# Optimization experiments

Measured on AMD Instinct MI355X. Metric: run time of the kernel, lower is better.

The kernel has to match this reference:

```python
import jax, jax.numpy as jnp
import numpy as np

N, E, F_IN = 12288, 196608, 1433


def setup_inputs() -> dict:
    key = jax.random.key(0)
    ks = jax.random.split(key, 11)
    inp = {
        "x": jax.random.normal(ks[0], (N, F_IN), dtype=jnp.float32),
        "edge_index": jax.random.randint(ks[1], (2, E), 0, N, dtype=jnp.int64),
        "W1": jax.random.normal(ks[2], (F_IN, 32), dtype=jnp.float32) * 0.02,
        "b1": jnp.zeros((32,), dtype=jnp.float32),
        "Wl": jax.random.normal(ks[3], (32, 16), dtype=jnp.float32) * 0.1,
        "bl": jnp.zeros((16,), dtype=jnp.float32),
        "Wr": jax.random.normal(ks[4], (32, 16), dtype=jnp.float32) * 0.1,
        "br": jnp.zeros((16,), dtype=jnp.float32),
        "W3": jax.random.normal(ks[5], (16, 7), dtype=jnp.float32) * 0.1,
        "b3": jnp.zeros((7,), dtype=jnp.float32),
    }
    return inp


def reference(x, edge_index, W1, b1, Wl, bl, Wr, br, W3, b3):
    n = x.shape[0]
    loops = jnp.arange(n, dtype=edge_index.dtype)
    row = jnp.concatenate([edge_index[0], loops])  # [E+N]
    col = jnp.concatenate([edge_index[1], loops])

    # ---- GCN layer: dense symmetric-normalized adjacency (faithful to original) ----
    # degree computed over the col index of self-looped edges
    deg = jnp.zeros((n,), dtype=x.dtype).at[col].add(1.0)
    dis = jnp.where(deg > 0, deg ** -0.5, 0.0)  # inf -> 0 guard
    A = jnp.zeros((n, n), dtype=x.dtype).at[row, col].add(1.0)  # dense A-hat
    A_norm = dis[:, None] * A * dis[None, :]  # D^-1/2 A D^-1/2
    h = (A_norm @ x) @ W1 + b1
    h = jax.nn.relu(h)  # [N, 32]

    # ---- GraphSAGE layer: mean over neighbors j with edge (i -> j) ----
    src, dst = edge_index[0], edge_index[1]
    agg_sum = jax.ops.segment_sum(h[dst], src, num_segments=n)  # [N, 32]
    cnt = jax.ops.segment_sum(jnp.ones((src.shape[0],), dtype=h.dtype), src, num_segments=n)
    agg = jnp.where(cnt[:, None] > 0, agg_sum / jnp.maximum(cnt, 1.0)[:, None], 0.0)
    out = jax.nn.relu(h @ Wl + bl + agg @ Wr + br)  # [N, 16]
    out = out / (jnp.linalg.norm(out, axis=1, keepdims=True) + 1e-6)

    # ---- head: linear + dropout(eval: identity) + softmax ----
    logits = out @ W3 + b3  # [N, 7]
    return jax.nn.softmax(logits, axis=1)
```

## Files before the change

### kernel.cpp

```cpp
#include <hip/hip_runtime.h>
#include <hip/hip_bf16.h>
#include <math.h>

#define GN 12288
#define GE 196608
#define GK 1433
#define GC 32
#define CAP 64
#define NGRP 192
#define GEMMB 768
#define EDGEB 768
#define PACKB 24
#define ZEROB 96
#define XSTR2 260

typedef __attribute__((ext_vector_type(8))) short bf16x8;
typedef __attribute__((ext_vector_type(4))) float f32x4;
typedef float f32x4a __attribute__((ext_vector_type(4), aligned(4)));

static __device__ inline unsigned short f2bf(float f) {
    unsigned u = __float_as_uint(f);
    return (unsigned short)((u + 0x7fffu + ((u >> 16) & 1u)) >> 16);
}
static __device__ inline float bf2f(unsigned short h) {
    return __uint_as_float(((unsigned)h) << 16);
}
static __device__ inline unsigned short f2bf_hw(float f) {
    return __builtin_bit_cast(unsigned short, __float2bfloat16(f));
}

__global__ __launch_bounds__(256) void prep_kernel(const float* __restrict__ W1,
                                                   unsigned* __restrict__ zbuf,
                                                   unsigned short* __restrict__ Whb,
                                                   unsigned short* __restrict__ Wlb) {
    int t = threadIdx.x, b = blockIdx.x;
    if (b < PACKB) {
        int idx = b * 256 + t;
        int g = idx >> 5, c = idx & 31;
        bf16x8 vh, vl;
        #pragma unroll
        for (int j = 0; j < 8; ++j) {
            int k = g * 8 + j;
            float f = (k < GK) ? W1[(size_t)k * GC + c] : 0.f;
            unsigned short hh = f2bf(f);
            vh[j] = (short)hh;
            vl[j] = (short)f2bf(f - bf2f(hh));
        }
        *(bf16x8*)(Whb + (size_t)idx * 8) = vh;
        *(bf16x8*)(Wlb + (size_t)idx * 8) = vl;
    } else {
        int idx = (b - PACKB) * 256 + t;
        zbuf[idx] = 0u;
    }
}

__global__ __launch_bounds__(256) void fused_kernel(const float* __restrict__ x,
                                                    const int* __restrict__ ei,
                                                    const unsigned short* __restrict__ Whb,
                                                    const unsigned short* __restrict__ Wlb,
                                                    float* __restrict__ xw,
                                                    unsigned* __restrict__ cnt,
                                                    unsigned* __restrict__ deg,
                                                    unsigned* __restrict__ adjF) {
    int t = threadIdx.x, bid = blockIdx.x;

    if (bid >= GEMMB) {
        int e = (bid - GEMMB) * 256 + t;
        int src = ei[e];
        int dst = ei[GE + e];
        unsigned pos = atomicAdd(&cnt[src], 1u);
        if (pos < CAP) adjF[(unsigned)src * CAP + pos] = (unsigned)dst;
        atomicAdd(&deg[dst], 1u);
        return;
    }

    __shared__ __align__(16) float smem[2 * 16 * XSTR2];
    float (*xs)[16][XSTR2] = (float (*)[16][XSTR2])smem;
    int lane = t & 63, w = t >> 6;
    int quad = lane >> 4, l15 = lane & 15;
    const float* xb = x + (size_t)bid * 16 * GK;
    f32x4 acc0 = {}, acc1 = {};
    int r0w = t >> 6;
    int posc = t & 63;
    f32x4 gA0, gA1, gA2, gA3, gB0, gB1, gB2, gB3;

#define LOADG(G0, G1, G2, G3, S) { \
    const float* pp = xb + (size_t)r0w * GK + (S) * 256 + posc * 4; \
    G0 = *(const f32x4a*)(pp); \
    G1 = *(const f32x4a*)(pp + 4 * GK); \
    G2 = *(const f32x4a*)(pp + 8 * GK); \
    G3 = *(const f32x4a*)(pp + 12 * GK); }

#define LG1(DST, ROFF, PP, KB) { \
    const float* q_ = (PP) + (size_t)(ROFF) * GK; \
    if ((KB) + 4 <= GK) DST = *(const f32x4a*)q_; \
    else { \
        DST[0] = ((KB) + 0 < GK) ? q_[0] : 0.f; \
        DST[1] = ((KB) + 1 < GK) ? q_[1] : 0.f; \
        DST[2] = ((KB) + 2 < GK) ? q_[2] : 0.f; \
        DST[3] = ((KB) + 3 < GK) ? q_[3] : 0.f; } }

#define LOADGT(G0, G1, G2, G3, S) { \
    const float* pp = xb + (size_t)r0w * GK + (S) * 256 + posc * 4; \
    int kb = (S) * 256 + posc * 4; \
    LG1(G0, 0, pp, kb)  LG1(G1, 4, pp, kb)  LG1(G2, 8, pp, kb)  LG1(G3, 12, pp, kb) }

#define STOREL(G0, G1, G2, G3, BUF) { \
    float* lp = &xs[BUF][r0w][posc * 4]; \
    *(f32x4*)(lp)               = G0; \
    *(f32x4*)(lp + 4 * XSTR2)   = G1; \
    *(f32x4*)(lp + 8 * XSTR2)   = G2; \
    *(f32x4*)(lp + 12 * XSTR2)  = G3; }

#define COMPUTE(S, BUF) { \
    _Pragma("unroll") \
    for (int c = 0; c < 2; ++c) { \
        int kl = w * 64 + c * 32 + quad * 8; \
        const float* ap = &xs[BUF][l15][kl]; \
        f32x4 x0 = *(const f32x4*)ap; \
        f32x4 x1 = *(const f32x4*)(ap + 4); \
        bf16x8 ah, al; \
        _Pragma("unroll") for (int j = 0; j < 4; ++j) { \
            unsigned short hh = f2bf_hw(x0[j]); \
            ah[j] = (short)hh; al[j] = (short)f2bf_hw(x0[j] - bf2f(hh)); } \
        _Pragma("unroll") for (int j = 0; j < 4; ++j) { \
            unsigned short hh = f2bf_hw(x1[j]); \
            ah[4 + j] = (short)hh; al[4 + j] = (short)f2bf_hw(x1[j] - bf2f(hh)); } \
        int gg = (S) * 32 + w * 8 + c * 4 + quad; \
        bf16x8 H0 = *(const bf16x8*)(Whb + (size_t)gg * 256 + l15 * 8); \
        bf16x8 H1 = *(const bf16x8*)(Whb + (size_t)gg * 256 + 128 + l15 * 8); \
        bf16x8 L0 = *(const bf16x8*)(Wlb + (size_t)gg * 256 + l15 * 8); \
        bf16x8 L1 = *(const bf16x8*)(Wlb + (size_t)gg * 256 + 128 + l15 * 8); \
        acc0 = __builtin_amdgcn_mfma_f32_16x16x32_bf16(ah, H0, acc0, 0, 0, 0); \
        acc1 = __builtin_amdgcn_mfma_f32_16x16x32_bf16(ah, H1, acc1, 0, 0, 0); \
        acc0 = __builtin_amdgcn_mfma_f32_16x16x32_bf16(ah, L0, acc0, 0, 0, 0); \
        acc1 = __builtin_amdgcn_mfma_f32_16x16x32_bf16(ah, L1, acc1, 0, 0, 0); \
        acc0 = __builtin_amdgcn_mfma_f32_16x16x32_bf16(al, H0, acc0, 0, 0, 0); \
        acc1 = __builtin_amdgcn_mfma_f32_16x16x32_bf16(al, H1, acc1, 0, 0, 0); \
    } }

    LOADG(gA0, gA1, gA2, gA3, 0);
    STOREL(gA0, gA1, gA2, gA3, 0);
    LOADG(gB0, gB1, gB2, gB3, 1);
    __syncthreads();
    LOADG(gA0, gA1, gA2, gA3, 2);
    COMPUTE(0, 0);
    STOREL(gB0, gB1, gB2, gB3, 1);
    __syncthreads();
    LOADG(gB0, gB1, gB2, gB3, 3);
    COMPUTE(1, 1);
    STOREL(gA0, gA1, gA2, gA3, 0);
    __syncthreads();
    LOADG(gA0, gA1, gA2, gA3, 4);
    COMPUTE(2, 0);
    STOREL(gB0, gB1, gB2, gB3, 1);
    __syncthreads();
    LOADGT(gB0, gB1, gB2, gB3, 5);
    COMPUTE(3, 1);
    STOREL(gA0, gA1, gA2, gA3, 0);
    __syncthreads();
    COMPUTE(4, 0);
    STOREL(gB0, gB1, gB2, gB3, 1);
    __syncthreads();
    COMPUTE(5, 1);

    float (*red)[16][32] = (float (*)[16][32])smem;
    #pragma unroll
    for (int i = 0; i < 4; ++i) {
        red[w][quad * 4 + i][l15] = acc0[i];
        red[w][quad * 4 + i][16 + l15] = acc1[i];
    }
    __syncthreads();
    int rr0 = t >> 5, cc0 = t & 31;
    float s0 = red[0][rr0][cc0] + red[1][rr0][cc0] + red[2][rr0][cc0] + red[3][rr0][cc0];
    int rr1 = rr0 + 8;
    float s1 = red[0][rr1][cc0] + red[1][rr1][cc0] + red[2][rr1][cc0] + red[3][rr1][cc0];
    xw[(size_t)bid * 512 + t] = s0;
    xw[(size_t)bid * 512 + 256 + t] = s1;
}

__global__ __launch_bounds__(256) void gcn_kernel(const float* __restrict__ xw,
                                                  const unsigned* __restrict__ deg,
                                                  const unsigned* __restrict__ cnt,
                                                  const unsigned* __restrict__ adjF,
                                                  const float* __restrict__ b1,
                                                  float* __restrict__ h) {
    int w = threadIdx.x >> 6;
    int lane = threadIdx.x & 63;
    int i = blockIdx.x * 4 + w;
    int f = lane & 31, half = lane >> 5;
    unsigned cl = min(cnt[i], (unsigned)CAP);
    const unsigned* ai = adjF + (unsigned)i * CAP;
    float acc = 0.f;
    for (unsigned j = half; j < cl; j += 8) {
        unsigned lim = cl - 1;
        unsigned j1 = j + 2, j2 = j + 4, j3 = j + 6;
        unsigned d0 = ai[j];
        unsigned d1 = ai[min(j1, lim)];
        unsigned d2 = ai[min(j2, lim)];
        unsigned d3 = ai[min(j3, lim)];
        float m1 = j1 < cl ? 1.f : 0.f;
        float m2 = j2 < cl ? 1.f : 0.f;
        float m3 = j3 < cl ? 1.f : 0.f;
        acc += xw[(size_t)d0 * GC + f] * rsqrtf((float)(deg[d0] + 1u));
        acc += m1 * xw[(size_t)d1 * GC + f] * rsqrtf((float)(deg[d1] + 1u));
        acc += m2 * xw[(size_t)d2 * GC + f] * rsqrtf((float)(deg[d2] + 1u));
        acc += m3 * xw[(size_t)d3 * GC + f] * rsqrtf((float)(deg[d3] + 1u));
    }
    acc += __shfl_xor(acc, 32, 64);
    float disi = rsqrtf((float)(deg[i] + 1u));
    float v = b1[f] + disi * (disi * xw[(size_t)i * GC + f] + acc);
    if (half == 0) h[(size_t)i * GC + f] = fmaxf(v, 0.f);
}

__global__ __launch_bounds__(256) void sage_kernel(const float* __restrict__ h,
                                                   const unsigned* __restrict__ cnt,
                                                   const unsigned* __restrict__ adjF,
                                                   const float* __restrict__ Wl,
                                                   const float* __restrict__ bl,
                                                   const float* __restrict__ Wr,
                                                   const float* __restrict__ br,
                                                   const float* __restrict__ W3,
                                                   const float* __restrict__ b3,
                                                   float* __restrict__ out) {
    __shared__ float sh[4][64];
    __shared__ float so[4][16];
    int w = threadIdx.x >> 6, lane = threadIdx.x & 63;
    int i = blockIdx.x * 4 + w;
    int f = lane & 31, half = lane >> 5;
    unsigned ci = cnt[i];
    unsigned cl = min(ci, (unsigned)CAP);
    const unsigned* ai = adjF + (unsigned)i * CAP;
    float acc = 0.f;
    for (unsigned j = half; j < cl; j += 8) {
        unsigned lim = cl - 1;
        unsigned j1 = j + 2, j2 = j + 4, j3 = j + 6;
        unsigned d0 = ai[j];
        unsigned d1 = ai[min(j1, lim)];
        unsigned d2 = ai[min(j2, lim)];
        unsigned d3 = ai[min(j3, lim)];
        float m1 = j1 < cl ? 1.f : 0.f;
        float m2 = j2 < cl ? 1.f : 0.f;
        float m3 = j3 < cl ? 1.f : 0.f;
        acc += h[(size_t)d0 * GC + f];
        acc += m1 * h[(size_t)d1 * GC + f];
        acc += m2 * h[(size_t)d2 * GC + f];
        acc += m3 * h[(size_t)d3 * GC + f];
    }
    acc += __shfl_xor(acc, 32, 64);
    float agg = ci ? acc / (float)ci : 0.f;
    float hv = h[(size_t)i * GC + f];
    if (half == 0) { sh[w][f] = hv; sh[w][32 + f] = agg; }
    __syncthreads();
    int c = lane;
    float hid = 0.f;
    if (c < 16) {
        hid = bl[c] + br[c];
        #pragma unroll
        for (int ff = 0; ff < 32; ++ff)
            hid += sh[w][ff] * Wl[ff * 16 + c] + sh[w][32 + ff] * Wr[ff * 16 + c];
        hid = fmaxf(hid, 0.f);
    }
    float n2 = hid * hid;
    n2 += __shfl_xor(n2, 1, 64);
    n2 += __shfl_xor(n2, 2, 64);
    n2 += __shfl_xor(n2, 4, 64);
    n2 += __shfl_xor(n2, 8, 64);
    float o = hid / (sqrtf(n2) + 1e-6f);
    if (c < 16) so[w][c] = o;
    __syncthreads();
    float logit = -INFINITY;
    if (lane < 7) {
        logit = b3[lane];
        #pragma unroll
        for (int cc = 0; cc < 16; ++cc) logit += so[w][cc] * W3[cc * 7 + lane];
    }
    float m = logit;
    m = fmaxf(m, __shfl_xor(m, 1, 64));
    m = fmaxf(m, __shfl_xor(m, 2, 64));
    m = fmaxf(m, __shfl_xor(m, 4, 64));
    float e = expf(logit - m);
    float s = e;
    s += __shfl_xor(s, 1, 64);
    s += __shfl_xor(s, 2, 64);
    s += __shfl_xor(s, 4, 64);
    if (lane < 7) out[(size_t)i * 7 + lane] = e / s;
}

extern "C" void kernel_launch(void* const* d_in, const int* in_sizes, int n_in,
                              void* d_out, int out_size, void* d_ws, size_t ws_size,
                              hipStream_t stream) {
    const float* x  = (const float*)d_in[0];
    const int*   ei = (const int*)d_in[1];
    const float* W1 = (const float*)d_in[2];
    const float* b1 = (const float*)d_in[3];
    const float* Wl = (const float*)d_in[4];
    const float* bl = (const float*)d_in[5];
    const float* Wr = (const float*)d_in[6];
    const float* br = (const float*)d_in[7];
    const float* W3 = (const float*)d_in[8];
    const float* b3 = (const float*)d_in[9];
    float* out = (float*)d_out;

    char* ws = (char*)d_ws;
    const size_t S = (size_t)GN * GC * 4;
    float*    xw   = (float*)(ws);
    unsigned* cnt  = (unsigned*)(ws + S);
    unsigned* deg  = cnt + GN;
    float*    h    = (float*)(deg + GN);
    unsigned* adjF = (unsigned*)((char*)h + S);
    unsigned short* Whb = (unsigned short*)((char*)adjF + (size_t)GN * CAP * 4);
    unsigned short* Wlb = Whb + (size_t)NGRP * GC * 8;

    prep_kernel<<<PACKB + ZEROB, 256, 0, stream>>>(W1, cnt, Whb, Wlb);
    fused_kernel<<<GEMMB + EDGEB, 256, 0, stream>>>(x, ei, Whb, Wlb, xw, cnt, deg, adjF);
    gcn_kernel<<<GN / 4, 256, 0, stream>>>(xw, deg, cnt, adjF, b1, h);
    sage_kernel<<<GN / 4, 256, 0, stream>>>(h, cnt, adjF, Wl, bl, Wr, br, W3, b3, out);
}
```

Measured before the change: 153.6 us.

## Halve GEMM K-stage width to shrink LDS and deepen pipeline; memset counters

The x·W1 GEMM now streams K in 128-wide stages over 12 steps instead of 256-wide stages over 6 steps. Each thread holds two float4 registers per buffer instead of four, and the LDS tile shrinks by half. The aim is to cut shared memory and register pressure so more blocks fit on each CU and hide global-load latency better, at the cost of twice as many barriers. The counter zeroing moves from extra prep_kernel blocks to a hipMemsetAsync, which adds a separate stream operation.

```diff
diff --git a/kernel.cpp b/kernel.cpp
--- a/kernel.cpp
+++ b/kernel.cpp
@@ -11,8 +11,7 @@
 #define GEMMB 768
 #define EDGEB 768
 #define PACKB 24
-#define ZEROB 96
-#define XSTR2 260
+#define XSTR3 132
 
 typedef __attribute__((ext_vector_type(8))) short bf16x8;
 typedef __attribute__((ext_vector_type(4))) float f32x4;
@@ -30,28 +29,22 @@
 }
 
 __global__ __launch_bounds__(256) void prep_kernel(const float* __restrict__ W1,
-                                                   unsigned* __restrict__ zbuf,
                                                    unsigned short* __restrict__ Whb,
                                                    unsigned short* __restrict__ Wlb) {
     int t = threadIdx.x, b = blockIdx.x;
-    if (b < PACKB) {
-        int idx = b * 256 + t;
-        int g = idx >> 5, c = idx & 31;
-        bf16x8 vh, vl;
-        #pragma unroll
-        for (int j = 0; j < 8; ++j) {
-            int k = g * 8 + j;
-            float f = (k < GK) ? W1[(size_t)k * GC + c] : 0.f;
-            unsigned short hh = f2bf(f);
-            vh[j] = (short)hh;
-            vl[j] = (short)f2bf(f - bf2f(hh));
-        }
-        *(bf16x8*)(Whb + (size_t)idx * 8) = vh;
-        *(bf16x8*)(Wlb + (size_t)idx * 8) = vl;
-    } else {
-        int idx = (b - PACKB) * 256 + t;
-        zbuf[idx] = 0u;
-    }
+    int idx = b * 256 + t;
+    int g = idx >> 5, c = idx & 31;
+    bf16x8 vh, vl;
+    #pragma unroll
+    for (int j = 0; j < 8; ++j) {
+        int k = g * 8 + j;
+        float f = (k < GK) ? W1[(size_t)k * GC + c] : 0.f;
+        unsigned short hh = f2bf(f);
+        vh[j] = (short)hh;
+        vl[j] = (short)f2bf(f - bf2f(hh));
+    }
+    *(bf16x8*)(Whb + (size_t)idx * 8) = vh;
+    *(bf16x8*)(Wlb + (size_t)idx * 8) = vl;
 }
 
 __global__ __launch_bounds__(256) void fused_kernel(const float* __restrict__ x,
@@ -74,22 +67,20 @@
         return;
     }
 
-    __shared__ __align__(16) float smem[2 * 16 * XSTR2];
-    float (*xs)[16][XSTR2] = (float (*)[16][XSTR2])smem;
+    __shared__ __align__(16) float smem[2 * 16 * XSTR3];
+    float (*xs)[16][XSTR3] = (float (*)[16][XSTR3])smem;
     int lane = t & 63, w = t >> 6;
     int quad = lane >> 4, l15 = lane & 15;
     const float* xb = x + (size_t)bid * 16 * GK;
     f32x4 acc0 = {}, acc1 = {};
-    int r0w = t >> 6;
-    int posc = t & 63;
-    f32x4 gA0, gA1, gA2, gA3, gB0, gB1, gB2, gB3;
-
-#define LOADG(G0, G1, G2, G3, S) { \
-    const float* pp = xb + (size_t)r0w * GK + (S) * 256 + posc * 4; \
+    int row0 = t >> 5;
+    int posc = t & 31;
+    f32x4 gA0, gA1, gB0, gB1;
+
+#define LOADG(G0, G1, S) { \
+    const float* pp = xb + (size_t)row0 * GK + (S) * 128 + posc * 4; \
     G0 = *(const f32x4a*)(pp); \
-    G1 = *(const f32x4a*)(pp + 4 * GK); \
-    G2 = *(const f32x4a*)(pp + 8 * GK); \
-    G3 = *(const f32x4a*)(pp + 12 * GK); }
+    G1 = *(const f32x4a*)(pp + 8 * GK); }
 
 #define LG1(DST, ROFF, PP, KB) { \
     const float* q_ = (PP) + (size_t)(ROFF) * GK; \
@@ -100,70 +91,58 @@
         DST[2] = ((KB) + 2 < GK) ? q_[2] : 0.f; \
         DST[3] = ((KB) + 3 < GK) ? q_[3] : 0.f; } }
 
-#define LOADGT(G0, G1, G2, G3, S) { \
-    const float* pp = xb + (size_t)r0w * GK + (S) * 256 + posc * 4; \
-    int kb = (S) * 256 + posc * 4; \
-    LG1(G0, 0, pp, kb)  LG1(G1, 4, pp, kb)  LG1(G2, 8, pp, kb)  LG1(G3, 12, pp, kb) }
-
-#define STOREL(G0, G1, G2, G3, BUF) { \
-    float* lp = &xs[BUF][r0w][posc * 4]; \
-    *(f32x4*)(lp)               = G0; \
-    *(f32x4*)(lp + 4 * XSTR2)   = G1; \
-    *(f32x4*)(lp + 8 * XSTR2)   = G2; \
-    *(f32x4*)(lp + 12 * XSTR2)  = G3; }
+#define LOADGT(G0, G1, S) { \
+    const float* pp = xb + (size_t)row0 * GK + (S) * 128 + posc * 4; \
+    int kb = (S) * 128 + posc * 4; \
+    LG1(G0, 0, pp, kb)  LG1(G1, 8, pp, kb) }
+
+#define STOREL(G0, G1, BUF) { \
+    float* lp = &xs[BUF][row0][posc * 4]; \
+    *(f32x4*)(lp)              = G0; \
+    *(f32x4*)(lp + 8 * XSTR3)  = G1; }
 
 #define COMPUTE(S, BUF) { \
-    _Pragma("unroll") \
-    for (int c = 0; c < 2; ++c) { \
-        int kl = w * 64 + c * 32 + quad * 8; \
-        const float* ap = &xs[BUF][l15][kl]; \
-        f32x4 x0 = *(const f32x4*)ap; \
-        f32x4 x1 = *(const f32x4*)(ap + 4); \
-        bf16x8 ah, al; \
-        _Pragma("unroll") for (int j = 0; j < 4; ++j) { \
-            unsigned short hh = f2bf_hw(x0[j]); \
-            ah[j] = (short)hh; al[j] = (short)f2bf_hw(x0[j] - bf2f(hh)); } \
-        _Pragma("unroll") for (int j = 0; j < 4; ++j) { \
-            unsigned short hh = f2bf_hw(x1[j]); \
-            ah[4 + j] = (short)hh; al[4 + j] = (short)f2bf_hw(x1[j] - bf2f(hh)); } \
-        int gg = (S) * 32 + w * 8 + c * 4 + quad; \
-        bf16x8 H0 = *(const bf16x8*)(Whb + (size_t)gg * 256 + l15 * 8); \
-        bf16x8 H1 = *(const bf16x8*)(Whb + (size_t)gg * 256 + 128 + l15 * 8); \
-        bf16x8 L0 = *(const bf16x8*)(Wlb + (size_t)gg * 256 + l15 * 8); \
-        bf16x8 L1 = *(const bf16x8*)(Wlb + (size_t)gg * 256 + 128 + l15 * 8); \
-        acc0 = __builtin_amdgcn_mfma_f32_16x16x32_bf16(ah, H0, acc0, 0, 0, 0); \
-        acc1 = __builtin_amdgcn_mfma_f32_16x16x32_bf16(ah, H1, acc1, 0, 0, 0); \
-        acc0 = __builtin_amdgcn_mfma_f32_16x16x32_bf16(ah, L0, acc0, 0, 0, 0); \
-        acc1 = __builtin_amdgcn_mfma_f32_16x16x32_bf16(ah, L1, acc1, 0, 0, 0); \
-        acc0 = __builtin_amdgcn_mfma_f32_16x16x32_bf16(al, H0, acc0, 0, 0, 0); \
-        acc1 = __builtin_amdgcn_mfma_f32_16x16x32_bf16(al, H1, acc1, 0, 0, 0); \
-    } }
-
-    LOADG(gA0, gA1, gA2, gA3, 0);
-    STOREL(gA0, gA1, gA2, gA3, 0);
-    LOADG(gB0, gB1, gB2, gB3, 1);
-    __syncthreads();
-    LOADG(gA0, gA1, gA2, gA3, 2);
-    COMPUTE(0, 0);
-    STOREL(gB0, gB1, gB2, gB3, 1);
-    __syncthreads();
-    LOADG(gB0, gB1, gB2, gB3, 3);
-    COMPUTE(1, 1);
-    STOREL(gA0, gA1, gA2, gA3, 0);
-    __syncthreads();
-    LOADG(gA0, gA1, gA2, gA3, 4);
-    COMPUTE(2, 0);
-    STOREL(gB0, gB1, gB2, gB3, 1);
-    __syncthreads();
-    LOADGT(gB0, gB1, gB2, gB3, 5);
-    COMPUTE(3, 1);
-    STOREL(gA0, gA1, gA2, gA3, 0);
-    __syncthreads();
-    COMPUTE(4, 0);
-    STOREL(gB0, gB1, gB2, gB3, 1);
-    __syncthreads();
-    COMPUTE(5, 1);
-
+    int kl = w * 32 + quad * 8; \
+    const float* ap = &xs[BUF][l15][kl]; \
+    f32x4 x0 = *(const f32x4*)ap; \
+    f32x4 x1 = *(const f32x4*)(ap + 4); \
+    bf16x8 ah, al; \
+    _Pragma("unroll") for (int j = 0; j < 4; ++j) { \
+        unsigned short hh = f2bf_hw(x0[j]); \
+        ah[j] = (short)hh; al[j] = (short)f2bf_hw(x0[j] - bf2f(hh)); } \
+    _Pragma("unroll") for (int j = 0; j < 4; ++j) { \
+        unsigned short hh = f2bf_hw(x1[j]); \
+        ah[4 + j] = (short)hh; al[4 + j] = (short)f2bf_hw(x1[j] - bf2f(hh)); } \
+    int gg = (S) * 16 + w * 4 + quad; \
+    bf16x8 H0 = *(const bf16x8*)(Whb + (size_t)gg * 256 + l15 * 8); \
+    bf16x8 H1 = *(const bf16x8*)(Whb + (size_t)gg * 256 + 128 + l15 * 8); \
+    bf16x8 L0 = *(const bf16x8*)(Wlb + (size_t)gg * 256 + l15 * 8); \
+    bf16x8 L1 = *(const bf16x8*)(Wlb + (size_t)gg * 256 + 128 + l15 * 8); \
+    acc0 = __builtin_amdgcn_mfma_f32_16x16x32_bf16(ah, H0, acc0, 0, 0, 0); \
+    acc1 = __builtin_amdgcn_mfma_f32_16x16x32_bf16(ah, H1, acc1, 0, 0, 0); \
+    acc0 = __builtin_amdgcn_mfma_f32_16x16x32_bf16(ah, L0, acc0, 0, 0, 0); \
+    acc1 = __builtin_amdgcn_mfma_f32_16x16x32_bf16(ah, L1, acc1, 0, 0, 0); \
+    acc0 = __builtin_amdgcn_mfma_f32_16x16x32_bf16(al, H0, acc0, 0, 0, 0); \
+    acc1 = __builtin_amdgcn_mfma_f32_16x16x32_bf16(al, H1, acc1, 0, 0, 0); }
+
+    LOADG(gA0, gA1, 0);
+    STOREL(gA0, gA1, 0);
+    LOADG(gB0, gB1, 1);
+    __syncthreads();
+    LOADG(gA0, gA1, 2);   COMPUTE(0, 0);  STOREL(gB0, gB1, 1); __syncthreads();
+    LOADG(gB0, gB1, 3);   COMPUTE(1, 1);  STOREL(gA0, gA1, 0); __syncthreads();
+    LOADG(gA0, gA1, 4);   COMPUTE(2, 0);  STOREL(gB0, gB1, 1); __syncthreads();
+    LOADG(gB0, gB1, 5);   COMPUTE(3, 1);  STOREL(gA0, gA1, 0); __syncthreads();
+    LOADG(gA0, gA1, 6);   COMPUTE(4, 0);  STOREL(gB0, gB1, 1); __syncthreads();
+    LOADG(gB0, gB1, 7);   COMPUTE(5, 1);  STOREL(gA0, gA1, 0); __syncthreads();
+    LOADG(gA0, gA1, 8);   COMPUTE(6, 0);  STOREL(gB0, gB1, 1); __syncthreads();
+    LOADG(gB0, gB1, 9);   COMPUTE(7, 1);  STOREL(gA0, gA1, 0); __syncthreads();
+    LOADG(gA0, gA1, 10);  COMPUTE(8, 0);  STOREL(gB0, gB1, 1); __syncthreads();
+    LOADGT(gB0, gB1, 11); COMPUTE(9, 1);  STOREL(gA0, gA1, 0); __syncthreads();
+    COMPUTE(10, 0);       STOREL(gB0, gB1, 1); __syncthreads();
+    COMPUTE(11, 1);
+
+    __syncthreads();
     float (*red)[16][32] = (float (*)[16][32])smem;
     #pragma unroll
     for (int i = 0; i < 4; ++i) {
@@ -312,7 +291,8 @@
     unsigned short* Whb = (unsigned short*)((char*)adjF + (size_t)GN * CAP * 4);
     unsigned short* Wlb = Whb + (size_t)NGRP * GC * 8;
 
-    prep_kernel<<<PACKB + ZEROB, 256, 0, stream>>>(W1, cnt, Whb, Wlb);
+    hipMemsetAsync(ws + S, 0, 2 * (size_t)GN * 4, stream);
+    prep_kernel<<<PACKB, 256, 0, stream>>>(W1, Whb, Wlb);
     fused_kernel<<<GEMMB + EDGEB, 256, 0, stream>>>(x, ei, Whb, Wlb, xw, cnt, deg, adjF);
     gcn_kernel<<<GN / 4, 256, 0, stream>>>(xw, deg, cnt, adjF, b1, h);
     sage_kernel<<<GN / 4, 256, 0, stream>>>(h, cnt, adjF, Wl, bl, Wr, br, W3, b3, out);
```

Result: slower. 158.1 us (+2.9%).
